# Kernel tuning notes

Measured on AMD Instinct MI355X. Metric: run time of the kernel, lower is better.

The kernel has to match this reference:

```python
import jax, jax.numpy as jnp
import numpy as np

B, T, V, E, DH, H, M, W = 64, 50, 32000, 64, 128, 8, 256, 50


def setup_inputs() -> dict:
    key = jax.random.key(0)
    ks = jax.random.split(key, 18)
    sc = 0.02
    return {
        "x": jax.random.randint(ks[0], (B, T), 0, V),
        "tok_emb": jax.random.normal(ks[1], (V, E)) * sc,
        "pos_emb": jax.random.normal(ks[2], (W, E)) * sc,
        "Wq": jax.random.normal(ks[3], (H, E, DH)) * sc,
        "bq": jnp.zeros((H, DH)),
        "Wk": jax.random.normal(ks[4], (H, E, DH)) * sc,
        "bk": jnp.zeros((H, DH)),
        "Wv": jax.random.normal(ks[5], (H, E, DH)) * sc,
        "bv": jnp.zeros((H, DH)),
        "Wo": jax.random.normal(ks[6], (H * DH, E)) * sc,
        "bo": jnp.zeros((E,)),
        "W1": jax.random.normal(ks[7], (E, M)) * sc,
        "b1": jnp.zeros((M,)),
        "W2": jax.random.normal(ks[8], (M, E)) * sc,
        "b2": jnp.zeros((E,)),
        "Wf": jax.random.normal(ks[9], (E, V)) * sc,
        "bf": jnp.zeros((V,)),
    }


def reference(x, tok_emb, pos_emb, Wq, bq, Wk, bk, Wv, bv, Wo, bo, W1, b1, W2, b2, Wf, bf):
    b, t = x.shape
    h = tok_emb[x] + pos_emb[:t]  # [B,T,E]
    # batched per-head QKV projections (original loops over 8 heads)
    Q = jnp.einsum("bte,hed->bhtd", h, Wq) + bq[None, :, None, :]
    K = jnp.einsum("bte,hed->bhtd", h, Wk) + bk[None, :, None, :]
    Vv = jnp.einsum("bte,hed->bhtd", h, Wv) + bv[None, :, None, :]
    scores = jnp.einsum("bhtd,bhsd->bhts", Q, K) / (DH ** 0.5)
    # faithful to original: masked_fill(tril(scores) == 0, -inf)
    scores = jnp.where(jnp.tril(scores) == 0, -jnp.inf, scores)
    attn = jax.nn.softmax(scores, axis=-1)
    o = jnp.einsum("bhts,bhsd->bhtd", attn, Vv)
    o = o.transpose(0, 2, 1, 3).reshape(b, t, H * DH)  # concat heads
    a = o @ Wo + bo
    # NOTE: no residual connections in the original module
    m = jax.nn.gelu(a @ W1 + b1, approximate=False)
    y = m @ W2 + b2
    logits = y @ Wf + bf  # [B,T,V]
    return logits
```

## Files before the change

### kernel.cpp

```cpp
#include <hip/hip_runtime.h>
#include <math.h>

#define T_ 50
#define R_ 3200

using u16 = unsigned short;
typedef __attribute__((ext_vector_type(8))) __bf16 bf16x8;
typedef __attribute__((ext_vector_type(4))) float f32x4;

__device__ __forceinline__ float bf2f(u16 u) {
  union { unsigned int i; float f; } x; x.i = ((unsigned int)u) << 16; return x.f;
}
__device__ __forceinline__ u16 f2bf(float f) {
  union { float f; unsigned int i; } x; x.f = f;
  unsigned int r = x.i + 0x7FFFu + ((x.i >> 16) & 1u);
  return (u16)(r >> 16);
}
__device__ __forceinline__ void split2(float v, u16& hi, u16& lo) {
  hi = f2bf(v);
  lo = f2bf(v - bf2f(hi));
}
__device__ __forceinline__ float gelu_f(float v) {
  return 0.5f * v * (1.0f + erff(v * 0.70710678118654752f));
}

__global__ __launch_bounds__(256) void k_embed(const int* __restrict__ x,
    const float* __restrict__ tok, const float* __restrict__ pos,
    float* __restrict__ h) {
  int i = blockIdx.x * 256 + threadIdx.x;
  if (i >= R_ * 64) return;
  int row = i >> 6, e = i & 63;
  int t = row % T_;
  int v = x[row];
  h[i] = tok[(long)v * 64 + e] + pos[t * 64 + e];
}

__global__ __launch_bounds__(256) void k_pack(
    const float* __restrict__ Wq, const float* __restrict__ Wk, const float* __restrict__ Wv,
    const float* __restrict__ bq, const float* __restrict__ bk, const float* __restrict__ bv,
    const float* __restrict__ Wo, const float* __restrict__ W1, const float* __restrict__ W2,
    u16* __restrict__ WqkvTh, u16* __restrict__ WqkvTl, float* __restrict__ bqkv,
    u16* __restrict__ WoTh, u16* __restrict__ WoTl,
    u16* __restrict__ W1Th, u16* __restrict__ W1Tl,
    u16* __restrict__ W2Th, u16* __restrict__ W2Tl) {
  int i = blockIdx.x * 256 + threadIdx.x;
  const int S0 = 196608, S1 = 3072, S2 = 65536, S3 = 16384;
  if (i < S0) {
    int n = i >> 6, e = i & 63;
    int p = n >> 10, rem = n & 1023;
    int hh = rem >> 7, d = rem & 127;
    const float* W = (p == 0) ? Wq : ((p == 1) ? Wk : Wv);
    split2(W[hh * 8192 + e * 128 + d], WqkvTh[i], WqkvTl[i]);
    return;
  }
  i -= S0;
  if (i < S1) { int p = i >> 10, rem = i & 1023;
    const float* bb = (p == 0) ? bq : ((p == 1) ? bk : bv);
    bqkv[i] = bb[rem]; return; }
  i -= S1;
  if (i < S2) { int n = i >> 10, k = i & 1023;
    split2(Wo[k * 64 + n], WoTh[i], WoTl[i]); return; }
  i -= S2;
  if (i < S3) { int n = i >> 6, k = i & 63;
    split2(W1[k * 256 + n], W1Th[i], W1Tl[i]); return; }
  i -= S3;
  { int n = i >> 8, k = i & 255;
    split2(W2[k * 64 + n], W2Th[i], W2Tl[i]); }
}

__global__ __launch_bounds__(256) void k_transpose_wf(const float* __restrict__ Wf,
    u16* __restrict__ WfTh, u16* __restrict__ WfTl) {
  __shared__ __align__(16) float tile[64][68];
  int n0 = blockIdx.x * 64;
  for (int c = threadIdx.x; c < 1024; c += 256) {
    int k = c >> 4, ch = (c & 15) * 4;
    *(float4*)&tile[k][ch] = *(const float4*)&Wf[(long)k * 32000 + n0 + ch];
  }
  __syncthreads();
  for (int c = threadIdx.x; c < 1024; c += 256) {
    int n = c >> 4, ch = (c & 15) * 4;
    u16 th[4], tl[4];
#pragma unroll
    for (int j = 0; j < 4; ++j) split2(tile[ch + j][n], th[j], tl[j]);
    *(ushort4*)&WfTh[(long)(n0 + n) * 64 + ch] = *(ushort4*)th;
    *(ushort4*)&WfTl[(long)(n0 + n) * 64 + ch] = *(ushort4*)tl;
  }
}

__global__ __launch_bounds__(256) void k_attn(const float* __restrict__ QKV,
                                              float* __restrict__ O) {
  int bh = blockIdx.x;
  int b = bh >> 3, hd = bh & 7;
  __shared__ __align__(16) float Kl[T_][128];
  __shared__ __align__(16) float Vl[T_][128];
  const int tid = threadIdx.x, lane = tid & 63, wave = tid >> 6;
  const float* base = QKV + (long)b * T_ * 3072 + hd * 128;
  for (int c = tid; c < T_ * 32; c += 256) {
    int s = c >> 5, c4 = (c & 31) * 4;
    *(float4*)&Kl[s][c4] = *(const float4*)&base[(long)s * 3072 + 1024 + c4];
    *(float4*)&Vl[s][c4] = *(const float4*)&base[(long)s * 3072 + 2048 + c4];
  }
  __syncthreads();
  const float scale = 0.0883883476483184406f;
  for (int r = wave; r < T_; r += 4) {
    float q0 = base[(long)r * 3072 + lane];
    float q1 = base[(long)r * 3072 + 64 + lane];
    float sc = -INFINITY;
    for (int s = 0; s <= r; ++s) {
      float p = q0 * Kl[s][lane] + q1 * Kl[s][64 + lane];
      p += __shfl_xor(p, 32); p += __shfl_xor(p, 16); p += __shfl_xor(p, 8);
      p += __shfl_xor(p, 4);  p += __shfl_xor(p, 2);  p += __shfl_xor(p, 1);
      if (lane == s) sc = p * scale;
    }
    float mx = sc;
    mx = fmaxf(mx, __shfl_xor(mx, 32)); mx = fmaxf(mx, __shfl_xor(mx, 16));
    mx = fmaxf(mx, __shfl_xor(mx, 8));  mx = fmaxf(mx, __shfl_xor(mx, 4));
    mx = fmaxf(mx, __shfl_xor(mx, 2));  mx = fmaxf(mx, __shfl_xor(mx, 1));
    float e = expf(sc - mx);
    float sum = e;
    sum += __shfl_xor(sum, 32); sum += __shfl_xor(sum, 16); sum += __shfl_xor(sum, 8);
    sum += __shfl_xor(sum, 4);  sum += __shfl_xor(sum, 2);  sum += __shfl_xor(sum, 1);
    float pr = e / sum;
    float o0 = 0.f, o1 = 0.f;
    for (int s = 0; s <= r; ++s) {
      float p = __shfl(pr, s);
      o0 += p * Vl[s][lane];
      o1 += p * Vl[s][64 + lane];
    }
    long orow = ((long)b * T_ + r) * 1024 + hd * 128;
    O[orow + lane] = o0;
    O[orow + 64 + lane] = o1;
  }
}

template <int BN, int ACT>
__global__ __launch_bounds__(256) void k_gemm(
    const float* __restrict__ A, int lda,
    const u16* __restrict__ Bth, const u16* __restrict__ Btl,
    const float* __restrict__ bias, float* __restrict__ C, int ldc, int K) {
  constexpr int BM = 64, BK = 64;
  constexpr int TN = BN / 16;
  __shared__ __align__(16) u16 Ah[BM][BK + 8];
  __shared__ __align__(16) u16 Al[BM][BK + 8];
  __shared__ __align__(16) u16 Bh[BN][BK + 8];
  __shared__ __align__(16) u16 Bl[BN][BK + 8];
  const int m0 = blockIdx.x * BM;
  const int n0 = blockIdx.y * BN;
  const int tid = threadIdx.x;
  const int lane = tid & 63, wave = tid >> 6;
  const int ln = lane & 15, quad = lane >> 4;
  const int wm = wave * 16;
  f32x4 acc[TN];
#pragma unroll
  for (int tn = 0; tn < TN; ++tn)
#pragma unroll
    for (int i = 0; i < 4; ++i) acc[tn][i] = 0.f;

  for (int kk = 0; kk < K; kk += BK) {
    for (int c = tid; c < BM * 16; c += 256) {
      int r = c >> 4, c4 = (c & 15) * 4;
      float4 v = *(const float4*)&A[(long)(m0 + r) * lda + kk + c4];
      u16 th[4], tl[4];
      split2(v.x, th[0], tl[0]); split2(v.y, th[1], tl[1]);
      split2(v.z, th[2], tl[2]); split2(v.w, th[3], tl[3]);
      *(ushort4*)&Ah[r][c4] = *(ushort4*)th;
      *(ushort4*)&Al[r][c4] = *(ushort4*)tl;
    }
    for (int c = tid; c < BN * 8; c += 256) {
      int r = c >> 3, c8 = (c & 7) * 8;
      *(uint4*)&Bh[r][c8] = *(const uint4*)&Bth[(long)(n0 + r) * K + kk + c8];
      *(uint4*)&Bl[r][c8] = *(const uint4*)&Btl[(long)(n0 + r) * K + kk + c8];
    }
    __syncthreads();
#pragma unroll
    for (int ks = 0; ks < BK / 32; ++ks) {
      bf16x8 ah = *(const bf16x8*)&Ah[wm + ln][ks * 32 + quad * 8];
      bf16x8 al = *(const bf16x8*)&Al[wm + ln][ks * 32 + quad * 8];
#pragma unroll
      for (int tn = 0; tn < TN; ++tn) {
        bf16x8 bh = *(const bf16x8*)&Bh[tn * 16 + ln][ks * 32 + quad * 8];
        bf16x8 bl = *(const bf16x8*)&Bl[tn * 16 + ln][ks * 32 + quad * 8];
        acc[tn] = __builtin_amdgcn_mfma_f32_16x16x32_bf16(ah, bh, acc[tn], 0, 0, 0);
        acc[tn] = __builtin_amdgcn_mfma_f32_16x16x32_bf16(al, bh, acc[tn], 0, 0, 0);
        acc[tn] = __builtin_amdgcn_mfma_f32_16x16x32_bf16(ah, bl, acc[tn], 0, 0, 0);
      }
    }
    __syncthreads();
  }
#pragma unroll
  for (int tn = 0; tn < TN; ++tn) {
    int col = n0 + tn * 16 + ln;
    float bv = bias[col];
#pragma unroll
    for (int r = 0; r < 4; ++r) {
      float v = acc[tn][r] + bv;
      if (ACT) v = gelu_f(v);
      C[(long)(m0 + wm + quad * 4 + r) * ldc + col] = v;
    }
  }
}

extern "C" void kernel_launch(void* const* d_in, const int* in_sizes, int n_in,
                              void* d_out, int out_size, void* d_ws, size_t ws_size,
                              hipStream_t stream) {
  const int*   x   = (const int*)d_in[0];
  const float* tok = (const float*)d_in[1];
  const float* pos = (const float*)d_in[2];
  const float* Wq  = (const float*)d_in[3];
  const float* bq  = (const float*)d_in[4];
  const float* Wk  = (const float*)d_in[5];
  const float* bk  = (const float*)d_in[6];
  const float* Wv  = (const float*)d_in[7];
  const float* bv  = (const float*)d_in[8];
  const float* Wo  = (const float*)d_in[9];
  const float* bo  = (const float*)d_in[10];
  const float* W1  = (const float*)d_in[11];
  const float* b1  = (const float*)d_in[12];
  const float* W2  = (const float*)d_in[13];
  const float* b2  = (const float*)d_in[14];
  const float* Wf  = (const float*)d_in[15];
  const float* bfv = (const float*)d_in[16];

  char* ws = (char*)d_ws;
  float* h      = (float*)(ws + 0);
  float* QKV    = (float*)(ws + 819200);
  float* o      = (float*)(ws + 40140800);
  float* a      = (float*)(ws + 53248000);
  float* m      = (float*)(ws + 54067200);
  float* y      = (float*)(ws + 57344000);
  u16*  WqkvTh  = (u16*)(ws + 58163200);
  u16*  WqkvTl  = (u16*)(ws + 58556416);
  float* bqkv   = (float*)(ws + 58949632);
  u16*  WoTh    = (u16*)(ws + 58961920);
  u16*  WoTl    = (u16*)(ws + 59092992);
  u16*  W1Th    = (u16*)(ws + 59224064);
  u16*  W1Tl    = (u16*)(ws + 59256832);
  u16*  W2Th    = (u16*)(ws + 59289600);
  u16*  W2Tl    = (u16*)(ws + 59322368);
  u16*  WfTh    = (u16*)(ws + 59355136);
  u16*  WfTl    = (u16*)(ws + 63451136);
  float* out    = (float*)d_out;

  k_embed<<<dim3(800), 256, 0, stream>>>(x, tok, pos, h);
  k_pack<<<dim3(1164), 256, 0, stream>>>(Wq, Wk, Wv, bq, bk, bv, Wo, W1, W2,
      WqkvTh, WqkvTl, bqkv, WoTh, WoTl, W1Th, W1Tl, W2Th, W2Tl);
  k_transpose_wf<<<dim3(500), 256, 0, stream>>>(Wf, WfTh, WfTl);
  k_gemm<128, 0><<<dim3(50, 24), 256, 0, stream>>>(h, 64, WqkvTh, WqkvTl, bqkv, QKV, 3072, 64);
  k_attn<<<dim3(512), 256, 0, stream>>>(QKV, o);
  k_gemm<64, 0><<<dim3(50, 1), 256, 0, stream>>>(o, 1024, WoTh, WoTl, bo, a, 64, 1024);
  k_gemm<128, 1><<<dim3(50, 2), 256, 0, stream>>>(a, 64, W1Th, W1Tl, b1, m, 256, 64);
  k_gemm<64, 0><<<dim3(50, 1), 256, 0, stream>>>(m, 256, W2Th, W2Tl, b2, y, 64, 256);
  k_gemm<128, 0><<<dim3(50, 250), 256, 0, stream>>>(y, 64, WfTh, WfTl, bfv, out, 32000, 64);
}
```

Baseline: 736.6 us.

## Merge prep kernels, pre-split activations, use LDS-free GEMM and transposed-K attention

Merges embedding, weight packing and the Wf transpose into one prep kernel, cutting launches. Producers now write hi/lo bf16 split activations, so the GEMMs read pre-split operands straight from global memory into MFMA registers, with no LDS staging or barriers. Attention computes all 64 scores per lane from a transposed K tile in LDS instead of a shuffle reduction per key, and passes probabilities through LDS. The LDS-free GEMM depends on cache hits for operand reuse, and the final logits GEMM may suffer from uncoalesced 16-byte row loads.

```diff
diff --git a/kernel.cpp b/kernel.cpp
--- a/kernel.cpp
+++ b/kernel.cpp
@@ -24,54 +24,54 @@
   return 0.5f * v * (1.0f + erff(v * 0.70710678118654752f));
 }
 
-__global__ __launch_bounds__(256) void k_embed(const int* __restrict__ x,
-    const float* __restrict__ tok, const float* __restrict__ pos,
-    float* __restrict__ h) {
-  int i = blockIdx.x * 256 + threadIdx.x;
-  if (i >= R_ * 64) return;
-  int row = i >> 6, e = i & 63;
-  int t = row % T_;
-  int v = x[row];
-  h[i] = tok[(long)v * 64 + e] + pos[t * 64 + e];
-}
-
-__global__ __launch_bounds__(256) void k_pack(
+__global__ __launch_bounds__(256) void k_prep(
+    const int* __restrict__ x, const float* __restrict__ tok, const float* __restrict__ pos,
     const float* __restrict__ Wq, const float* __restrict__ Wk, const float* __restrict__ Wv,
     const float* __restrict__ bq, const float* __restrict__ bk, const float* __restrict__ bv,
     const float* __restrict__ Wo, const float* __restrict__ W1, const float* __restrict__ W2,
+    const float* __restrict__ Wf,
+    u16* __restrict__ hh, u16* __restrict__ hl,
     u16* __restrict__ WqkvTh, u16* __restrict__ WqkvTl, float* __restrict__ bqkv,
     u16* __restrict__ WoTh, u16* __restrict__ WoTl,
     u16* __restrict__ W1Th, u16* __restrict__ W1Tl,
-    u16* __restrict__ W2Th, u16* __restrict__ W2Tl) {
-  int i = blockIdx.x * 256 + threadIdx.x;
-  const int S0 = 196608, S1 = 3072, S2 = 65536, S3 = 16384;
-  if (i < S0) {
-    int n = i >> 6, e = i & 63;
-    int p = n >> 10, rem = n & 1023;
-    int hh = rem >> 7, d = rem & 127;
-    const float* W = (p == 0) ? Wq : ((p == 1) ? Wk : Wv);
-    split2(W[hh * 8192 + e * 128 + d], WqkvTh[i], WqkvTl[i]);
-    return;
-  }
-  i -= S0;
-  if (i < S1) { int p = i >> 10, rem = i & 1023;
-    const float* bb = (p == 0) ? bq : ((p == 1) ? bk : bv);
-    bqkv[i] = bb[rem]; return; }
-  i -= S1;
-  if (i < S2) { int n = i >> 10, k = i & 1023;
-    split2(Wo[k * 64 + n], WoTh[i], WoTl[i]); return; }
-  i -= S2;
-  if (i < S3) { int n = i >> 6, k = i & 63;
-    split2(W1[k * 256 + n], W1Th[i], W1Tl[i]); return; }
-  i -= S3;
-  { int n = i >> 8, k = i & 255;
-    split2(W2[k * 64 + n], W2Th[i], W2Tl[i]); }
-}
-
-__global__ __launch_bounds__(256) void k_transpose_wf(const float* __restrict__ Wf,
+    u16* __restrict__ W2Th, u16* __restrict__ W2Tl,
     u16* __restrict__ WfTh, u16* __restrict__ WfTl) {
   __shared__ __align__(16) float tile[64][68];
-  int n0 = blockIdx.x * 64;
+  int blk = blockIdx.x;
+  if (blk < 800) {
+    int i = blk * 256 + threadIdx.x;
+    int row = i >> 6, e = i & 63;
+    int t = row % T_;
+    split2(tok[(long)x[row] * 64 + e] + pos[t * 64 + e], hh[i], hl[i]);
+    return;
+  }
+  if (blk < 1964) {
+    int i = (blk - 800) * 256 + threadIdx.x;
+    const int S0 = 196608, S1 = 3072, S2 = 65536, S3 = 16384;
+    if (i < S0) {
+      int n = i >> 6, e = i & 63;
+      int p = n >> 10, rem = n & 1023;
+      int hh2 = rem >> 7, d = rem & 127;
+      const float* W = (p == 0) ? Wq : ((p == 1) ? Wk : Wv);
+      split2(W[hh2 * 8192 + e * 128 + d], WqkvTh[i], WqkvTl[i]);
+      return;
+    }
+    i -= S0;
+    if (i < S1) { int p = i >> 10, rem = i & 1023;
+      const float* bb = (p == 0) ? bq : ((p == 1) ? bk : bv);
+      bqkv[i] = bb[rem]; return; }
+    i -= S1;
+    if (i < S2) { int n = i >> 10, k = i & 1023;
+      split2(Wo[k * 64 + n], WoTh[i], WoTl[i]); return; }
+    i -= S2;
+    if (i < S3) { int n = i >> 6, k = i & 63;
+      split2(W1[k * 256 + n], W1Th[i], W1Tl[i]); return; }
+    i -= S3;
+    if (i < S3) { int n = i >> 8, k = i & 255;
+      split2(W2[k * 64 + n], W2Th[i], W2Tl[i]); }
+    return;
+  }
+  int n0 = (blk - 1964) * 64;
   for (int c = threadIdx.x; c < 1024; c += 256) {
     int k = c >> 4, ch = (c & 15) * 4;
     *(float4*)&tile[k][ch] = *(const float4*)&Wf[(long)k * 32000 + n0 + ch];
@@ -87,31 +87,88 @@
   }
 }
 
+template <int TN, int ACT, int SPLIT>
+__global__ __launch_bounds__(256) void k_gemm_rr(
+    const u16* __restrict__ Ah, const u16* __restrict__ Al,
+    const u16* __restrict__ Bh, const u16* __restrict__ Bl,
+    const float* __restrict__ bias, float* __restrict__ Cf,
+    u16* __restrict__ Ch, u16* __restrict__ Cl, int ldc, int K) {
+  const int m0 = blockIdx.x * 64;
+  const int n0 = blockIdx.y * (TN * 16);
+  const int lane = threadIdx.x & 63, wave = threadIdx.x >> 6;
+  const int ln = lane & 15, quad = lane >> 4;
+  const int wm = wave * 16;
+  f32x4 acc[TN];
+#pragma unroll
+  for (int tn = 0; tn < TN; ++tn)
+#pragma unroll
+    for (int i = 0; i < 4; ++i) acc[tn][i] = 0.f;
+
+  const long arow = (long)(m0 + wm + ln) * K;
+  for (int kk = 0; kk < K; kk += 64) {
+    const long ab = arow + kk + quad * 8;
+    bf16x8 a0h = *(const bf16x8*)&Ah[ab];
+    bf16x8 a1h = *(const bf16x8*)&Ah[ab + 32];
+    bf16x8 a0l = *(const bf16x8*)&Al[ab];
+    bf16x8 a1l = *(const bf16x8*)&Al[ab + 32];
+#pragma unroll
+    for (int tn = 0; tn < TN; ++tn) {
+      const long bb = (long)(n0 + tn * 16 + ln) * K + kk + quad * 8;
+      bf16x8 b0h = *(const bf16x8*)&Bh[bb];
+      bf16x8 b1h = *(const bf16x8*)&Bh[bb + 32];
+      bf16x8 b0l = *(const bf16x8*)&Bl[bb];
+      bf16x8 b1l = *(const bf16x8*)&Bl[bb + 32];
+      acc[tn] = __builtin_amdgcn_mfma_f32_16x16x32_bf16(a0h, b0h, acc[tn], 0, 0, 0);
+      acc[tn] = __builtin_amdgcn_mfma_f32_16x16x32_bf16(a0l, b0h, acc[tn], 0, 0, 0);
+      acc[tn] = __builtin_amdgcn_mfma_f32_16x16x32_bf16(a0h, b0l, acc[tn], 0, 0, 0);
+      acc[tn] = __builtin_amdgcn_mfma_f32_16x16x32_bf16(a1h, b1h, acc[tn], 0, 0, 0);
+      acc[tn] = __builtin_amdgcn_mfma_f32_16x16x32_bf16(a1l, b1h, acc[tn], 0, 0, 0);
+      acc[tn] = __builtin_amdgcn_mfma_f32_16x16x32_bf16(a1h, b1l, acc[tn], 0, 0, 0);
+    }
+  }
+#pragma unroll
+  for (int tn = 0; tn < TN; ++tn) {
+    int col = n0 + tn * 16 + ln;
+    float bv = bias[col];
+#pragma unroll
+    for (int r = 0; r < 4; ++r) {
+      long idx = (long)(m0 + wm + quad * 4 + r) * ldc + col;
+      float v = acc[tn][r] + bv;
+      if (ACT) v = gelu_f(v);
+      if (SPLIT) split2(v, Ch[idx], Cl[idx]);
+      else Cf[idx] = v;
+    }
+  }
+}
+
 __global__ __launch_bounds__(256) void k_attn(const float* __restrict__ QKV,
-                                              float* __restrict__ O) {
-  int bh = blockIdx.x;
-  int b = bh >> 3, hd = bh & 7;
-  __shared__ __align__(16) float Kl[T_][128];
-  __shared__ __align__(16) float Vl[T_][128];
+                                              u16* __restrict__ Oh,
+                                              u16* __restrict__ Ol) {
+  __shared__ float KT[128][65];
+  __shared__ __align__(16) float VL[T_][128];
+  __shared__ float PL[4][64];
+  const int b = blockIdx.x >> 3, hd = blockIdx.x & 7;
   const int tid = threadIdx.x, lane = tid & 63, wave = tid >> 6;
   const float* base = QKV + (long)b * T_ * 3072 + hd * 128;
-  for (int c = tid; c < T_ * 32; c += 256) {
-    int s = c >> 5, c4 = (c & 31) * 4;
-    *(float4*)&Kl[s][c4] = *(const float4*)&base[(long)s * 3072 + 1024 + c4];
-    *(float4*)&Vl[s][c4] = *(const float4*)&base[(long)s * 3072 + 2048 + c4];
+  for (int c = tid; c < T_ * 128; c += 256) {
+    int s = c >> 7, d = c & 127;
+    KT[d][s] = base[(long)s * 3072 + 1024 + d];
+    VL[s][d] = base[(long)s * 3072 + 2048 + d];
   }
   __syncthreads();
   const float scale = 0.0883883476483184406f;
   for (int r = wave; r < T_; r += 4) {
-    float q0 = base[(long)r * 3072 + lane];
-    float q1 = base[(long)r * 3072 + 64 + lane];
-    float sc = -INFINITY;
-    for (int s = 0; s <= r; ++s) {
-      float p = q0 * Kl[s][lane] + q1 * Kl[s][64 + lane];
-      p += __shfl_xor(p, 32); p += __shfl_xor(p, 16); p += __shfl_xor(p, 8);
-      p += __shfl_xor(p, 4);  p += __shfl_xor(p, 2);  p += __shfl_xor(p, 1);
-      if (lane == s) sc = p * scale;
-    }
+    const float* qrow = base + (long)r * 3072;
+    float ac0 = 0.f, ac1 = 0.f, ac2 = 0.f, ac3 = 0.f;
+#pragma unroll 4
+    for (int d = 0; d < 128; d += 4) {
+      float4 q = *(const float4*)&qrow[d];
+      ac0 += q.x * KT[d][lane];
+      ac1 += q.y * KT[d + 1][lane];
+      ac2 += q.z * KT[d + 2][lane];
+      ac3 += q.w * KT[d + 3][lane];
+    }
+    float sc = (lane <= r) ? (ac0 + ac1 + ac2 + ac3) * scale : -INFINITY;
     float mx = sc;
     mx = fmaxf(mx, __shfl_xor(mx, 32)); mx = fmaxf(mx, __shfl_xor(mx, 16));
     mx = fmaxf(mx, __shfl_xor(mx, 8));  mx = fmaxf(mx, __shfl_xor(mx, 4));
@@ -120,83 +177,16 @@
     float sum = e;
     sum += __shfl_xor(sum, 32); sum += __shfl_xor(sum, 16); sum += __shfl_xor(sum, 8);
     sum += __shfl_xor(sum, 4);  sum += __shfl_xor(sum, 2);  sum += __shfl_xor(sum, 1);
-    float pr = e / sum;
+    PL[wave][lane] = e / sum;
     float o0 = 0.f, o1 = 0.f;
     for (int s = 0; s <= r; ++s) {
-      float p = __shfl(pr, s);
-      o0 += p * Vl[s][lane];
-      o1 += p * Vl[s][64 + lane];
+      float p = PL[wave][s];
+      o0 += p * VL[s][lane];
+      o1 += p * VL[s][64 + lane];
     }
     long orow = ((long)b * T_ + r) * 1024 + hd * 128;
-    O[orow + lane] = o0;
-    O[orow + 64 + lane] = o1;
-  }
-}
-
-template <int BN, int ACT>
-__global__ __launch_bounds__(256) void k_gemm(
-    const float* __restrict__ A, int lda,
-    const u16* __restrict__ Bth, const u16* __restrict__ Btl,
-    const float* __restrict__ bias, float* __restrict__ C, int ldc, int K) {
-  constexpr int BM = 64, BK = 64;
-  constexpr int TN = BN / 16;
-  __shared__ __align__(16) u16 Ah[BM][BK + 8];
-  __shared__ __align__(16) u16 Al[BM][BK + 8];
-  __shared__ __align__(16) u16 Bh[BN][BK + 8];
-  __shared__ __align__(16) u16 Bl[BN][BK + 8];
-  const int m0 = blockIdx.x * BM;
-  const int n0 = blockIdx.y * BN;
-  const int tid = threadIdx.x;
-  const int lane = tid & 63, wave = tid >> 6;
-  const int ln = lane & 15, quad = lane >> 4;
-  const int wm = wave * 16;
-  f32x4 acc[TN];
-#pragma unroll
-  for (int tn = 0; tn < TN; ++tn)
-#pragma unroll
-    for (int i = 0; i < 4; ++i) acc[tn][i] = 0.f;
-
-  for (int kk = 0; kk < K; kk += BK) {
-    for (int c = tid; c < BM * 16; c += 256) {
-      int r = c >> 4, c4 = (c & 15) * 4;
-      float4 v = *(const float4*)&A[(long)(m0 + r) * lda + kk + c4];
-      u16 th[4], tl[4];
-      split2(v.x, th[0], tl[0]); split2(v.y, th[1], tl[1]);
-      split2(v.z, th[2], tl[2]); split2(v.w, th[3], tl[3]);
-      *(ushort4*)&Ah[r][c4] = *(ushort4*)th;
-      *(ushort4*)&Al[r][c4] = *(ushort4*)tl;
-    }
-    for (int c = tid; c < BN * 8; c += 256) {
-      int r = c >> 3, c8 = (c & 7) * 8;
-      *(uint4*)&Bh[r][c8] = *(const uint4*)&Bth[(long)(n0 + r) * K + kk + c8];
-      *(uint4*)&Bl[r][c8] = *(const uint4*)&Btl[(long)(n0 + r) * K + kk + c8];
-    }
-    __syncthreads();
-#pragma unroll
-    for (int ks = 0; ks < BK / 32; ++ks) {
-      bf16x8 ah = *(const bf16x8*)&Ah[wm + ln][ks * 32 + quad * 8];
-      bf16x8 al = *(const bf16x8*)&Al[wm + ln][ks * 32 + quad * 8];
-#pragma unroll
-      for (int tn = 0; tn < TN; ++tn) {
-        bf16x8 bh = *(const bf16x8*)&Bh[tn * 16 + ln][ks * 32 + quad * 8];
-        bf16x8 bl = *(const bf16x8*)&Bl[tn * 16 + ln][ks * 32 + quad * 8];
-        acc[tn] = __builtin_amdgcn_mfma_f32_16x16x32_bf16(ah, bh, acc[tn], 0, 0, 0);
-        acc[tn] = __builtin_amdgcn_mfma_f32_16x16x32_bf16(al, bh, acc[tn], 0, 0, 0);
-        acc[tn] = __builtin_amdgcn_mfma_f32_16x16x32_bf16(ah, bl, acc[tn], 0, 0, 0);
-      }
-    }
-    __syncthreads();
-  }
-#pragma unroll
-  for (int tn = 0; tn < TN; ++tn) {
-    int col = n0 + tn * 16 + ln;
-    float bv = bias[col];
-#pragma unroll
-    for (int r = 0; r < 4; ++r) {
-      float v = acc[tn][r] + bv;
-      if (ACT) v = gelu_f(v);
-      C[(long)(m0 + wm + quad * 4 + r) * ldc + col] = v;
-    }
+    split2(o0, Oh[orow + lane], Ol[orow + lane]);
+    split2(o1, Oh[orow + 64 + lane], Ol[orow + 64 + lane]);
   }
 }
 
@@ -222,33 +212,44 @@
   const float* bfv = (const float*)d_in[16];
 
   char* ws = (char*)d_ws;
-  float* h      = (float*)(ws + 0);
-  float* QKV    = (float*)(ws + 819200);
-  float* o      = (float*)(ws + 40140800);
-  float* a      = (float*)(ws + 53248000);
-  float* m      = (float*)(ws + 54067200);
-  float* y      = (float*)(ws + 57344000);
-  u16*  WqkvTh  = (u16*)(ws + 58163200);
-  u16*  WqkvTl  = (u16*)(ws + 58556416);
-  float* bqkv   = (float*)(ws + 58949632);
-  u16*  WoTh    = (u16*)(ws + 58961920);
-  u16*  WoTl    = (u16*)(ws + 59092992);
-  u16*  W1Th    = (u16*)(ws + 59224064);
-  u16*  W1Tl    = (u16*)(ws + 59256832);
-  u16*  W2Th    = (u16*)(ws + 59289600);
-  u16*  W2Tl    = (u16*)(ws + 59322368);
-  u16*  WfTh    = (u16*)(ws + 59355136);
-  u16*  WfTl    = (u16*)(ws + 63451136);
+  size_t off = 0;
+  auto alloc = [&](size_t bytes) { char* p = ws + off; off += (bytes + 255) & ~(size_t)255; return p; };
+  u16*   hh     = (u16*)alloc(409600);
+  u16*   hl     = (u16*)alloc(409600);
+  float* QKV    = (float*)alloc(39321600);
+  u16*   oh     = (u16*)alloc(6553600);
+  u16*   ol     = (u16*)alloc(6553600);
+  u16*   ah     = (u16*)alloc(409600);
+  u16*   al     = (u16*)alloc(409600);
+  u16*   mh     = (u16*)alloc(1638400);
+  u16*   ml     = (u16*)alloc(1638400);
+  u16*   yh     = (u16*)alloc(409600);
+  u16*   yl     = (u16*)alloc(409600);
+  u16*   WqkvTh = (u16*)alloc(393216);
+  u16*   WqkvTl = (u16*)alloc(393216);
+  float* bqkv   = (float*)alloc(12288);
+  u16*   WoTh   = (u16*)alloc(131072);
+  u16*   WoTl   = (u16*)alloc(131072);
+  u16*   W1Th   = (u16*)alloc(32768);
+  u16*   W1Tl   = (u16*)alloc(32768);
+  u16*   W2Th   = (u16*)alloc(32768);
+  u16*   W2Tl   = (u16*)alloc(32768);
+  u16*   WfTh   = (u16*)alloc(4096000);
+  u16*   WfTl   = (u16*)alloc(4096000);
   float* out    = (float*)d_out;
 
-  k_embed<<<dim3(800), 256, 0, stream>>>(x, tok, pos, h);
-  k_pack<<<dim3(1164), 256, 0, stream>>>(Wq, Wk, Wv, bq, bk, bv, Wo, W1, W2,
-      WqkvTh, WqkvTl, bqkv, WoTh, WoTl, W1Th, W1Tl, W2Th, W2Tl);
-  k_transpose_wf<<<dim3(500), 256, 0, stream>>>(Wf, WfTh, WfTl);
-  k_gemm<128, 0><<<dim3(50, 24), 256, 0, stream>>>(h, 64, WqkvTh, WqkvTl, bqkv, QKV, 3072, 64);
-  k_attn<<<dim3(512), 256, 0, stream>>>(QKV, o);
-  k_gemm<64, 0><<<dim3(50, 1), 256, 0, stream>>>(o, 1024, WoTh, WoTl, bo, a, 64, 1024);
-  k_gemm<128, 1><<<dim3(50, 2), 256, 0, stream>>>(a, 64, W1Th, W1Tl, b1, m, 256, 64);
-  k_gemm<64, 0><<<dim3(50, 1), 256, 0, stream>>>(m, 256, W2Th, W2Tl, b2, y, 64, 256);
-  k_gemm<128, 0><<<dim3(50, 250), 256, 0, stream>>>(y, 64, WfTh, WfTl, bfv, out, 32000, 64);
-}
+  k_prep<<<dim3(2464), 256, 0, stream>>>(x, tok, pos, Wq, Wk, Wv, bq, bk, bv,
+      Wo, W1, W2, Wf, hh, hl, WqkvTh, WqkvTl, bqkv, WoTh, WoTl,
+      W1Th, W1Tl, W2Th, W2Tl, WfTh, WfTl);
+  k_gemm_rr<8, 0, 0><<<dim3(50, 24), 256, 0, stream>>>(
+      hh, hl, WqkvTh, WqkvTl, bqkv, QKV, nullptr, nullptr, 3072, 64);
+  k_attn<<<dim3(512), 256, 0, stream>>>(QKV, oh, ol);
+  k_gemm_rr<4, 0, 1><<<dim3(50, 1), 256, 0, stream>>>(
+      oh, ol, WoTh, WoTl, bo, nullptr, ah, al, 64, 1024);
+  k_gemm_rr<8, 1, 1><<<dim3(50, 2), 256, 0, stream>>>(
+      ah, al, W1Th, W1Tl, b1, nullptr, mh, ml, 256, 64);
+  k_gemm_rr<4, 0, 1><<<dim3(50, 1), 256, 0, stream>>>(
+      mh, ml, W2Th, W2Tl, b2, nullptr, yh, yl, 64, 256);
+  k_gemm_rr<8, 0, 0><<<dim3(50, 250), 256, 0, stream>>>(
+      yh, yl, WfTh, WfTl, bfv, out, nullptr, nullptr, 32000, 64);
+}
```

After: 745.3 us. Within noise of the previous version (+1.2%).
